# Kernel tuning notes

Hardware: AMD Instinct MI355X
Metric: run time of the kernel (lower is better)

Reference implementation:

```python
import jax, jax.numpy as jnp
import numpy as np

B, N, D, H, C = 32, 512, 256, 256, 2
EPS_NEIGH = 0.3
VSN = 1e-12
SMOOTH_R, DEGREE_R, SPARSITY_R = 0.2, 0.0, 0.1


def setup_inputs() -> dict:
    key = jax.random.key(0)
    ks = jax.random.split(key, 12)
    s = 0.02
    return {
        "context": jax.random.normal(ks[0], (B, N, D), jnp.float32),
        "attention_mask": jnp.ones((B, N, 1), jnp.int32),
        "W_gcn": jax.random.normal(ks[1], (D, H), jnp.float32) * s,
        "b_gcn": jnp.zeros((H,), jnp.float32),
        "W_att1": jax.random.normal(ks[2], (H, H), jnp.float32) * s,
        "b_att1": jnp.zeros((H,), jnp.float32),
        "ln_g": jnp.ones((H,), jnp.float32),
        "ln_b": jnp.zeros((H,), jnp.float32),
        "W_att2": jax.random.normal(ks[3], (H, 1), jnp.float32) * s,
        "b_att2": jnp.zeros((1,), jnp.float32),
        "W_out": jax.random.normal(ks[4], (H, C), jnp.float32) * s,
        "b_out": jnp.zeros((C,), jnp.float32),
    }


def reference(context, attention_mask, W_gcn, b_gcn, W_att1, b_att1,
              ln_g, ln_b, W_att2, b_att2, W_out, b_out):
    # --- GraphLearner (cosine metric + epsilon neighbourhood) ---
    cn = context / jnp.maximum(
        jnp.linalg.norm(context, axis=-1, keepdims=True), VSN)
    att = jnp.einsum('bnd,bmd->bnm', cn, cn)              # [B,N,N]
    mask = jax.lax.stop_gradient((att > EPS_NEIGH).astype(att.dtype))
    adj = att * mask                                      # markoff_value = 0

    # --- GCN diffusion (row-normalized adjacency) ---
    row = adj.sum(-1, keepdims=True)                      # [B,N,1]
    adj_norm = adj / (row + VSN)
    h = jax.nn.relu(
        jnp.einsum('bnm,bmd->bnd', adj_norm, context) @ W_gcn + b_gcn)

    # --- AttentionNetPooling: Linear -> LayerNorm -> GELU -> Linear(1) ---
    a = h @ W_att1 + b_att1
    mu = a.mean(-1, keepdims=True)
    var = a.var(-1, keepdims=True)
    a = (a - mu) / jnp.sqrt(var + 1e-5) * ln_g + ln_b
    w = jax.nn.gelu(a, approximate=False) @ W_att2 + b_att2   # [B,N,1]
    w = jnp.where(attention_mask == 0, -jnp.inf, w)
    w = jax.nn.softmax(w, axis=1)
    pooled = jnp.sum(w * h, axis=1)                       # [B,H]
    logits = pooled @ W_out + b_out                       # [B,C]

    # --- add_batch_graph_loss (L = diag(rowsum) - adj, topk = N) ---
    Lx = row * context - jnp.einsum('bnm,bmd->bnd', adj, context)
    smooth = SMOOTH_R * jnp.mean(
        jnp.sum(context * Lx, axis=(-1, -2)) / (N * N))
    deg = -DEGREE_R * jnp.mean(
        jnp.sum(jnp.log(row[..., 0] + VSN), axis=-1) / N)
    sparsity = SPARSITY_R * jnp.sum(adj ** 2) / (N * N) / B
    graph_loss = smooth + deg + sparsity
    return logits, graph_loss
```

## Files before the change

kernel.cpp:

```cpp
#include <hip/hip_runtime.h>
#include <math.h>

#define NS 512
#define ND 256
#define LIST_CAP 32768u

typedef short short8 __attribute__((ext_vector_type(8)));
typedef float f32x16 __attribute__((ext_vector_type(16)));

__device__ __forceinline__ unsigned short bf16_rne(float x) {
  unsigned u = __float_as_uint(x);
  unsigned r = u + 0x7fffu + ((u >> 16) & 1u);
  return (unsigned short)(r >> 16);
}
__device__ __forceinline__ float bf16_tof(unsigned short h) {
  return __uint_as_float(((unsigned)h) << 16);
}
__device__ __forceinline__ void bsplit(float x, unsigned short& h, unsigned short& l) {
  h = bf16_rne(x);
  l = bf16_rne(x - bf16_tof(h));
}
__device__ __forceinline__ float wave_sum(float v) {
  v += __shfl_xor(v, 1);  v += __shfl_xor(v, 2);  v += __shfl_xor(v, 4);
  v += __shfl_xor(v, 8);  v += __shfl_xor(v, 16); v += __shfl_xor(v, 32);
  return v;
}


__device__ __forceinline__ void gload_lds16(const void* g, void* l) {
  __builtin_amdgcn_global_load_lds(
      (const __attribute__((address_space(1))) unsigned int*)g,
      (__attribute__((address_space(3))) unsigned int*)l, 16, 0, 0);
}

__device__ __forceinline__ void stage4(const unsigned short* __restrict__ hiA,
                                       const unsigned short* __restrict__ loA, int grA,
                                       const unsigned short* __restrict__ hiB,
                                       const unsigned short* __restrict__ loB, int grB,
                                       int k0, char* lds, int wid, int lane)
{
  #pragma unroll
  for (int q = 0; q < 2; ++q) {
    const int c = (q * 4 + wid) * 64 + lane;
    const int row = c >> 3;
    const int soff = ((c & 7) * 16) ^ ((row & 7) << 4);
    const int dest = (q * 4 + wid) * 1024;
    const size_t ga = (size_t)(grA + row) * ND + k0 + (soff >> 1);
    const size_t gb = (size_t)(grB + row) * ND + k0 + (soff >> 1);
    gload_lds16(hiA + ga, lds + dest);
    gload_lds16(loA + ga, lds + 8192 + dest);
    gload_lds16(hiB + gb, lds + 16384 + dest);
    gload_lds16(loB + gb, lds + 24576 + dest);
  }
}

#define SWZB(row, off) (((row) << 7) + (((off) ^ (((row) & 7) << 4))))

#define STEP_MFMA(lds, arow, brow) do { \
  _Pragma("unroll") \
  for (int ks = 0; ks < 4; ++ks) { \
    const int off = ks * 32 + hl * 16; \
    short8 ah = *(const short8*)((lds) + SWZB((arow), off)); \
    short8 al = *(const short8*)((lds) + 8192 + SWZB((arow), off)); \
    short8 bh = *(const short8*)((lds) + 16384 + SWZB((brow), off)); \
    short8 bl = *(const short8*)((lds) + 24576 + SWZB((brow), off)); \
    acc = __builtin_amdgcn_mfma_f32_32x32x16_bf16(ah, bh, acc, 0, 0, 0); \
    acc = __builtin_amdgcn_mfma_f32_32x32x16_bf16(ah, bl, acc, 0, 0, 0); \
    acc = __builtin_amdgcn_mfma_f32_32x32x16_bf16(al, bh, acc, 0, 0, 0); \
  } \
} while (0)

__global__ __launch_bounds__(256)
void k_prep(const float* __restrict__ ctx, const float* __restrict__ Wg,
            const float* __restrict__ Wa,
            float* __restrict__ nrm, float* __restrict__ nsq,
            unsigned short* __restrict__ cnhi, unsigned short* __restrict__ cnlo,
            unsigned short* __restrict__ wgthi, unsigned short* __restrict__ wgtlo,
            unsigned short* __restrict__ wathi, unsigned short* __restrict__ watlo,
            unsigned* __restrict__ cnt)
{
  if (blockIdx.x >= 4096) {
    int wb = blockIdx.x - 4096;
    int j = wb & 255, selA = wb >> 8;
    int k = threadIdx.x;
    if (wb == 0 && k == 0) *cnt = 0u;
    const float* W = selA ? Wa : Wg;
    unsigned short h, l;
    bsplit(W[k * ND + j], h, l);
    if (selA) { wathi[j * ND + k] = h; watlo[j * ND + k] = l; }
    else      { wgthi[j * ND + k] = h; wgtlo[j * ND + k] = l; }
    return;
  }
  int w = threadIdx.x >> 6, lane = threadIdx.x & 63;
  int g = blockIdx.x * 4 + w;
  float4 v = ((const float4*)ctx)[(size_t)g * 64 + lane];
  float ss = v.x*v.x + v.y*v.y + v.z*v.z + v.w*v.w;
  ss = wave_sum(ss);
  float n = sqrtf(ss);
  float rn = 1.f / fmaxf(n, 1e-12f);
  if (lane == 0) { nrm[g] = n; nsq[g] = ss; }
  ushort4 hi, lo;
  bsplit(v.x * rn, hi.x, lo.x);
  bsplit(v.y * rn, hi.y, lo.y);
  bsplit(v.z * rn, hi.z, lo.z);
  bsplit(v.w * rn, hi.w, lo.w);
  ((ushort4*)cnhi)[(size_t)g * 64 + lane] = hi;
  ((ushort4*)cnlo)[(size_t)g * 64 + lane] = lo;
}

__global__ __launch_bounds__(256, 4)
void k_gram2(const unsigned short* __restrict__ cnhi, const unsigned short* __restrict__ cnlo,
             const float* __restrict__ nrm,
             float* __restrict__ rowp, float* __restrict__ diag,
             float* __restrict__ pA2, float* __restrict__ pA3,
             unsigned* __restrict__ cnt, unsigned* __restrict__ keys,
             float* __restrict__ vals)
{
  __shared__ __align__(16) char lds[32768];
  __shared__ float s_row[2][64];
  __shared__ float s_col[2][64];
  __shared__ float sred[8];
  const int bx0 = blockIdx.x;
  const int bx = (bx0 & 7) * 144 + (bx0 >> 3);
  const int b = bx / 36;
  int rem = bx % 36, ti = 0;
  #pragma unroll
  for (int q = 0; q < 7; ++q) { if (rem >= 8 - ti) { rem -= 8 - ti; ++ti; } }
  const int tj = ti + rem;
  const bool diagT = (ti == tj);
  const int i0 = ti * 64, j0 = tj * 64;
  const int bB = b * NS;
  const int rbA = bB + i0, rbB = bB + j0;

  const int tid = threadIdx.x;
  const int lane = tid & 63, wid = tid >> 6;
  const int l31 = lane & 31, hl = lane >> 5;
  const int wr = wid >> 1, wc = wid & 1;
  const int arow = wr * 32 + l31;
  const int brow = wc * 32 + l31;

  f32x16 acc = {};
  #pragma unroll
  for (int t = 0; t < 4; ++t) {
    stage4(cnhi, cnlo, rbA, cnhi, cnlo, rbB, t * 64, lds, wid, lane);
    __syncthreads();
    STEP_MFMA(lds, arow, brow);
    __syncthreads();
  }

  const float nc = nrm[rbB + wc * 32 + l31];
  const int gcol = wc * 32 + l31;
  float a2 = 0.f, a3 = 0.f, colsum = 0.f;

  #pragma unroll
  for (int r = 0; r < 16; ++r) {
    const int rofs = (r & 3) + 8 * (r >> 2) + 4 * hl;
    const int grow = wr * 32 + rofs;
    const float nr = nrm[rbA + grow];
    float v = acc[r];
    float adj = (v > 0.3f) ? v : 0.f;
    float q2 = adj * adj;
    a3 += q2;
    a2 += q2 * nr * nc;
    colsum += adj;
    if (diagT) {
      if (grow == gcol) {
        diag[bB + i0 + grow] = adj;
      } else if (adj > 0.f) {
        unsigned idx = atomicAdd(cnt, 1u);
        if (idx < LIST_CAP) {
          keys[idx] = (unsigned)((bB + i0 + grow) * NS + (j0 + gcol));
          vals[idx] = adj;
        }
      }
    } else if (adj > 0.f) {
      unsigned idx = atomicAdd(cnt, 2u);
      if (idx < LIST_CAP) {
        keys[idx] = (unsigned)((bB + i0 + grow) * NS + (j0 + gcol));
        vals[idx] = adj;
      }
      if (idx + 1u < LIST_CAP) {
        keys[idx + 1u] = (unsigned)((bB + j0 + gcol) * NS + (i0 + grow));
        vals[idx + 1u] = adj;
      }
    }
    float rs = adj;
    rs += __shfl_xor(rs, 1); rs += __shfl_xor(rs, 2); rs += __shfl_xor(rs, 4);
    rs += __shfl_xor(rs, 8); rs += __shfl_xor(rs, 16);
    if (l31 == 0) s_row[wc][grow] = rs;
  }
  colsum += __shfl_xor(colsum, 32);
  if (!diagT && hl == 0) s_col[wr][gcol] = colsum;
  a2 = wave_sum(a2);
  a3 = wave_sum(a3);
  if (lane == 0) { sred[wid] = a2; sred[4 + wid] = a3; }
  __syncthreads();
  if (tid < 64) {
    rowp[tj * 16384 + rbA + tid] = s_row[0][tid] + s_row[1][tid];
    if (!diagT)
      rowp[ti * 16384 + rbB + tid] = s_col[0][tid] + s_col[1][tid];
  }
  if (tid == 0) {
    float f = diagT ? 1.f : 2.f;
    pA2[bx] = f * (sred[0] + sred[1] + sred[2] + sred[3]);
    pA3[bx] = f * (sred[4] + sred[5] + sred[6] + sred[7]);
  }
}

__global__ __launch_bounds__(256)
void k_mrow(const float* __restrict__ ctx, const float* __restrict__ rowp,
            const float* __restrict__ nsq, const float* __restrict__ diag,
            const unsigned* __restrict__ cnt, const unsigned* __restrict__ keys,
            const float* __restrict__ vals,
            unsigned short* __restrict__ Mhi, unsigned short* __restrict__ Mlo,
            float* __restrict__ pA1)
{
  __shared__ float sa[4];
  int tid = threadIdx.x, w = tid >> 6, lane = tid & 63;
  int g = blockIdx.x * 4 + w;
  float r = 0.f;
  #pragma unroll
  for (int s = 0; s < 8; ++s) r += rowp[s * 16384 + g];
  float rr = 1.f / (r + 1e-12f);
  float4 v = ((const float4*)ctx)[(size_t)g * 64 + lane];
  float s = diag[g] * rr;
  float mx = v.x * s, my = v.y * s, mz = v.z * s, mw = v.w * s;
  unsigned c = *cnt; if (c > LIST_CAP) c = LIST_CAP;
  for (unsigned e = 0; e < c; ++e) {
    unsigned key = keys[e];
    if ((key >> 9) == (unsigned)g) {
      float vv = vals[e] * rr;
      unsigned bm = ((unsigned)g & ~511u) | (key & 511u);
      float4 cv = ((const float4*)ctx)[(size_t)bm * 64 + lane];
      mx = fmaf(vv, cv.x, mx); my = fmaf(vv, cv.y, my);
      mz = fmaf(vv, cv.z, mz); mw = fmaf(vv, cv.w, mw);
    }
  }
  ushort4 hi, lo;
  bsplit(mx, hi.x, lo.x); bsplit(my, hi.y, lo.y);
  bsplit(mz, hi.z, lo.z); bsplit(mw, hi.w, lo.w);
  ((ushort4*)Mhi)[(size_t)g * 64 + lane] = hi;
  ((ushort4*)Mlo)[(size_t)g * 64 + lane] = lo;
  if (lane == 0) sa[w] = r * nsq[g];
  __syncthreads();
  if (tid == 0) pA1[blockIdx.x] = sa[0] + sa[1] + sa[2] + sa[3];
}

template<int MODE>
__global__ __launch_bounds__(256, 4)
void k_mm(const unsigned short* __restrict__ Ahi, const unsigned short* __restrict__ Alo,
          const unsigned short* __restrict__ Bthi, const unsigned short* __restrict__ Btlo,
          const float* __restrict__ bias, float* __restrict__ outf,
          unsigned short* __restrict__ Ohi, unsigned short* __restrict__ Olo)
{
  __shared__ __align__(16) char lds[32768];
  const int i0 = blockIdx.x * 64;
  const int c0 = blockIdx.y * 64;
  const int tid = threadIdx.x;
  const int lane = tid & 63, wid = tid >> 6;
  const int l31 = lane & 31, hl = lane >> 5;
  const int wr = wid >> 1, wc = wid & 1;
  const int arow = wr * 32 + l31;
  const int brow = wc * 32 + l31;

  f32x16 acc = {};
  #pragma unroll
  for (int t = 0; t < 4; ++t) {
    stage4(Ahi, Alo, i0, Bthi, Btlo, c0, t * 64, lds, wid, lane);
    __syncthreads();
    STEP_MFMA(lds, arow, brow);
    __syncthreads();
  }

  const int gcol = c0 + wc * 32 + l31;
  const float bv = bias[gcol];
  #pragma unroll
  for (int r = 0; r < 16; ++r) {
    const int rofs = (r & 3) + 8 * (r >> 2) + 4 * hl;
    const size_t grow = (size_t)(i0 + wr * 32 + rofs);
    float v = acc[r] + bv;
    if (MODE == 0) {
      v = fmaxf(v, 0.f);
      unsigned short h, l;
      bsplit(v, h, l);
      Ohi[grow * ND + gcol] = h;
      Olo[grow * ND + gcol] = l;
    } else {
      outf[grow * ND + gcol] = v;
    }
  }
}

__global__ __launch_bounds__(256)
void k_ln(const float* __restrict__ a, const float* __restrict__ g,
          const float* __restrict__ bt, const float* __restrict__ W2,
          const float* __restrict__ b2, float* __restrict__ wl)
{
  int w = threadIdx.x >> 6, lane = threadIdx.x & 63;
  int row = blockIdx.x * 4 + w;
  float4 x = ((const float4*)a)[(size_t)row * 64 + lane];
  float s = x.x + x.y + x.z + x.w;
  float ss = fmaf(x.x, x.x, fmaf(x.y, x.y, fmaf(x.z, x.z, x.w * x.w)));
  s = wave_sum(s); ss = wave_sum(ss);
  float mu = s * (1.f / 256.f);
  float var = ss * (1.f / 256.f) - mu * mu;
  float rstd = rsqrtf(fmaxf(var, 0.f) + 1e-5f);
  float4 gg = ((const float4*)g)[lane];
  float4 bb = ((const float4*)bt)[lane];
  float4 wv = ((const float4*)W2)[lane];
  const float inv_sqrt2 = 0.70710678118654752f;
  float d = 0.f;
  float y = (x.x - mu) * rstd * gg.x + bb.x;
  d = fmaf(0.5f * y * (1.f + erff(y * inv_sqrt2)), wv.x, d);
  y = (x.y - mu) * rstd * gg.y + bb.y;
  d = fmaf(0.5f * y * (1.f + erff(y * inv_sqrt2)), wv.y, d);
  y = (x.z - mu) * rstd * gg.z + bb.z;
  d = fmaf(0.5f * y * (1.f + erff(y * inv_sqrt2)), wv.z, d);
  y = (x.w - mu) * rstd * gg.w + bb.w;
  d = fmaf(0.5f * y * (1.f + erff(y * inv_sqrt2)), wv.w, d);
  d = wave_sum(d);
  if (lane == 0) wl[row] = d + b2[0];
}

__global__ __launch_bounds__(256)
void k_pool2(const float* __restrict__ wl, const int* __restrict__ amask,
             const unsigned short* __restrict__ hhi, const unsigned short* __restrict__ hlo,
             float* __restrict__ part)
{
  __shared__ float sw[512];
  __shared__ float red[256];
  int b = blockIdx.x >> 4, p = blockIdx.x & 15, t = threadIdx.x;
  float l0 = (amask[b * NS + t]       == 0) ? -INFINITY : wl[b * NS + t];
  float l1 = (amask[b * NS + 256 + t] == 0) ? -INFINITY : wl[b * NS + 256 + t];
  red[t] = fmaxf(l0, l1);
  __syncthreads();
  for (int s = 128; s; s >>= 1) { if (t < s) red[t] = fmaxf(red[t], red[t + s]); __syncthreads(); }
  float mx = red[0];
  __syncthreads();
  float e0 = expf(l0 - mx), e1 = expf(l1 - mx);
  red[t] = e0 + e1;
  __syncthreads();
  for (int s = 128; s; s >>= 1) { if (t < s) red[t] += red[t + s]; __syncthreads(); }
  float inv = 1.f / red[0];
  sw[t] = e0 * inv; sw[256 + t] = e1 * inv;
  __syncthreads();
  const size_t base = (size_t)b * NS * ND + (size_t)p * 32 * ND + t;
  float acc = 0.f;
  #pragma unroll 8
  for (int n = 0; n < 32; ++n) {
    float hv = bf16_tof(hhi[base + (size_t)n * ND]) + bf16_tof(hlo[base + (size_t)n * ND]);
    acc = fmaf(sw[p * 32 + n], hv, acc);
  }
  part[(size_t)blockIdx.x * ND + t] = acc;
}

__global__ __launch_bounds__(256)
void k_final(const float* __restrict__ part, const float* __restrict__ W_out,
             const float* __restrict__ b_out, const float* __restrict__ pA1,
             const float* __restrict__ pA2, const float* __restrict__ pA3,
             float* __restrict__ out)
{
  __shared__ float red[512];
  int t = threadIdx.x;
  if (blockIdx.x < 32) {
    int b = blockIdx.x;
    float pl = 0.f;
    #pragma unroll
    for (int p = 0; p < 16; ++p) pl += part[(size_t)(b * 16 + p) * ND + t];
    red[t]       = pl * W_out[t * 2 + 0];
    red[256 + t] = pl * W_out[t * 2 + 1];
    __syncthreads();
    for (int s = 128; s; s >>= 1) {
      if (t < s) { red[t] += red[t + s]; red[256 + t] += red[256 + t + s]; }
      __syncthreads();
    }
    if (t == 0) {
      out[b * 2 + 0] = red[0]   + b_out[0];
      out[b * 2 + 1] = red[256] + b_out[1];
    }
  } else {
    float r1 = 0.f;
    #pragma unroll
    for (int i = 0; i < 16; ++i) r1 += pA1[i * 256 + t];
    float r2 = 0.f, r3 = 0.f;
    #pragma unroll
    for (int i = 0; i < 5; ++i) {
      int idx = i * 256 + t;
      if (idx < 1152) { r2 += pA2[idx]; r3 += pA3[idx]; }
    }
    red[t] = r1; red[256 + t] = r2;
    __syncthreads();
    for (int s = 128; s; s >>= 1) {
      if (t < s) { red[t] += red[t + s]; red[256 + t] += red[256 + t + s]; }
      __syncthreads();
    }
    r1 = red[0]; r2 = red[256];
    __syncthreads();
    red[t] = r3;
    __syncthreads();
    for (int s = 128; s; s >>= 1) { if (t < s) red[t] += red[t + s]; __syncthreads(); }
    if (t == 0) {
      float smooth = 0.2f * (r1 - r2) * (1.f / (32.f * 512.f * 512.f));
      float spars  = 0.1f * red[0] * (1.f / (512.f * 512.f)) * (1.f / 32.f);
      out[64] = smooth + spars;
    }
  }
}

extern "C" void kernel_launch(void* const* d_in, const int* in_sizes, int n_in,
                              void* d_out, int out_size, void* d_ws, size_t ws_size,
                              hipStream_t stream)
{
  (void)in_sizes; (void)n_in; (void)out_size; (void)ws_size;
  const float* ctx    = (const float*)d_in[0];
  const int*   amask  = (const int*)d_in[1];
  const float* W_gcn  = (const float*)d_in[2];
  const float* b_gcn  = (const float*)d_in[3];
  const float* W_att1 = (const float*)d_in[4];
  const float* b_att1 = (const float*)d_in[5];
  const float* ln_g   = (const float*)d_in[6];
  const float* ln_b   = (const float*)d_in[7];
  const float* W_att2 = (const float*)d_in[8];
  const float* b_att2 = (const float*)d_in[9];
  const float* W_out  = (const float*)d_in[10];
  const float* b_out  = (const float*)d_in[11];
  float* out = (float*)d_out;

  float* ws = (float*)d_ws;
  unsigned short* cnhi = (unsigned short*)ws;
  unsigned short* cnlo = (unsigned short*)(ws + 2097152);
  unsigned short* hhi  = cnhi;
  unsigned short* hlo  = cnlo;
  float* part = ws + 4194304;
  unsigned short* Mhi = (unsigned short*)(ws + 8388608);
  unsigned short* Mlo = (unsigned short*)(ws + 8388608 + 2097152);
  float* abuf = ws + 8388608;
  float* sp   = ws + 12582912;
  float* nrm  = sp;            sp += 16384;
  float* nsq  = sp;            sp += 16384;
  float* rowp = sp;            sp += 131072;
  float* diag = sp;            sp += 16384;
  float* wl   = sp;            sp += 16384;
  float* pA1  = sp;            sp += 4096;
  float* pA2  = sp;            sp += 1280;
  float* pA3  = sp;            sp += 1280;
  unsigned* cnt  = (unsigned*)sp;  sp += 64;
  unsigned* keys = (unsigned*)sp;  sp += 32768;
  float* vals = sp;            sp += 32768;
  unsigned short* wgthi = (unsigned short*)sp; sp += 32768;
  unsigned short* wgtlo = (unsigned short*)sp; sp += 32768;
  unsigned short* wathi = (unsigned short*)sp; sp += 32768;
  unsigned short* watlo = (unsigned short*)sp; sp += 32768;

  k_prep<<<4608, 256, 0, stream>>>(ctx, W_gcn, W_att1, nrm, nsq, cnhi, cnlo,
                                   wgthi, wgtlo, wathi, watlo, cnt);
  k_gram2<<<1152, 256, 0, stream>>>(cnhi, cnlo, nrm, rowp, diag, pA2, pA3,
                                    cnt, keys, vals);
  k_mrow<<<4096, 256, 0, stream>>>(ctx, rowp, nsq, diag, cnt, keys, vals,
                                   Mhi, Mlo, pA1);
  k_mm<0><<<dim3(256, 4), 256, 0, stream>>>(Mhi, Mlo, wgthi, wgtlo, b_gcn,
                                            nullptr, hhi, hlo);
  k_mm<1><<<dim3(256, 4), 256, 0, stream>>>(hhi, hlo, wathi, watlo, b_att1,
                                            abuf, nullptr, nullptr);
  k_ln<<<4096, 256, 0, stream>>>(abuf, ln_g, ln_b, W_att2, b_att2, wl);
  k_pool2<<<512, 256, 0, stream>>>(wl, amask, hhi, hlo, part);
  k_final<<<33, 256, 0, stream>>>(part, W_out, b_out, pA1, pA2, pA3, out);
}
```

Baseline: 84.88 us.

## Fuse diffusion into GCN GEMM, fuse attention GEMM with LayerNorm, merge pooling

The separate row-mixing kernel is removed. The GCN GEMM now runs directly on the normalized context and scales each row by norm*diag/rowsum, relying on the adjacency being diagonal-dominant. Rows that have off-diagonal neighbours are recomputed exactly in the attention kernel with a scalar dot-product fixup. The attention Linear, LayerNorm, GELU and Linear(1) are fused into one kernel using a pre-swizzled W_att1 fragment layout, and pooling is merged with the final reduction. Together these cut five launches and intermediate buffers down to three kernels. The costs are a serial, quadratic scan of the neighbour list in every attention block and a pooling stage with only 33 blocks.

```diff
diff --git a/kernel.cpp b/kernel.cpp
--- a/kernel.cpp
+++ b/kernel.cpp
@@ -25,7 +25,6 @@
   v += __shfl_xor(v, 8);  v += __shfl_xor(v, 16); v += __shfl_xor(v, 32);
   return v;
 }
-
 
 __device__ __forceinline__ void gload_lds16(const void* g, void* l) {
   __builtin_amdgcn_global_load_lds(
@@ -70,13 +69,23 @@
   } \
 } while (0)
 
+__device__ __forceinline__ float pdot_raw(const float* __restrict__ ctx,
+                                          const float* __restrict__ Wg,
+                                          int row, int t) {
+  const float* cr = ctx + (size_t)row * ND;
+  float a = 0.f;
+  #pragma unroll 4
+  for (int k = 0; k < ND; ++k) a = fmaf(cr[k], Wg[(size_t)k * ND + t], a);
+  return a;
+}
+
 __global__ __launch_bounds__(256)
 void k_prep(const float* __restrict__ ctx, const float* __restrict__ Wg,
             const float* __restrict__ Wa,
             float* __restrict__ nrm, float* __restrict__ nsq,
             unsigned short* __restrict__ cnhi, unsigned short* __restrict__ cnlo,
             unsigned short* __restrict__ wgthi, unsigned short* __restrict__ wgtlo,
-            unsigned short* __restrict__ wathi, unsigned short* __restrict__ watlo,
+            unsigned short* __restrict__ wfhi, unsigned short* __restrict__ wflo,
             unsigned* __restrict__ cnt)
 {
   if (blockIdx.x >= 4096) {
@@ -84,11 +93,15 @@
     int j = wb & 255, selA = wb >> 8;
     int k = threadIdx.x;
     if (wb == 0 && k == 0) *cnt = 0u;
-    const float* W = selA ? Wa : Wg;
     unsigned short h, l;
-    bsplit(W[k * ND + j], h, l);
-    if (selA) { wathi[j * ND + k] = h; watlo[j * ND + k] = l; }
-    else      { wgthi[j * ND + k] = h; wgtlo[j * ND + k] = l; }
+    if (selA) {
+      bsplit(Wa[k * ND + j], h, l);
+      int idx = ((((k >> 4) * 8) + (j >> 5)) * 64 + ((k >> 3) & 1) * 32 + (j & 31)) * 8 + (k & 7);
+      wfhi[idx] = h; wflo[idx] = l;
+    } else {
+      bsplit(Wg[k * ND + j], h, l);
+      wgthi[j * ND + k] = h; wgtlo[j * ND + k] = l;
+    }
     return;
   }
   int w = threadIdx.x >> 6, lane = threadIdx.x & 63;
@@ -207,53 +220,17 @@
   }
 }
 
-__global__ __launch_bounds__(256)
-void k_mrow(const float* __restrict__ ctx, const float* __restrict__ rowp,
-            const float* __restrict__ nsq, const float* __restrict__ diag,
-            const unsigned* __restrict__ cnt, const unsigned* __restrict__ keys,
-            const float* __restrict__ vals,
-            unsigned short* __restrict__ Mhi, unsigned short* __restrict__ Mlo,
-            float* __restrict__ pA1)
-{
-  __shared__ float sa[4];
-  int tid = threadIdx.x, w = tid >> 6, lane = tid & 63;
-  int g = blockIdx.x * 4 + w;
-  float r = 0.f;
-  #pragma unroll
-  for (int s = 0; s < 8; ++s) r += rowp[s * 16384 + g];
-  float rr = 1.f / (r + 1e-12f);
-  float4 v = ((const float4*)ctx)[(size_t)g * 64 + lane];
-  float s = diag[g] * rr;
-  float mx = v.x * s, my = v.y * s, mz = v.z * s, mw = v.w * s;
-  unsigned c = *cnt; if (c > LIST_CAP) c = LIST_CAP;
-  for (unsigned e = 0; e < c; ++e) {
-    unsigned key = keys[e];
-    if ((key >> 9) == (unsigned)g) {
-      float vv = vals[e] * rr;
-      unsigned bm = ((unsigned)g & ~511u) | (key & 511u);
-      float4 cv = ((const float4*)ctx)[(size_t)bm * 64 + lane];
-      mx = fmaf(vv, cv.x, mx); my = fmaf(vv, cv.y, my);
-      mz = fmaf(vv, cv.z, mz); mw = fmaf(vv, cv.w, mw);
-    }
-  }
-  ushort4 hi, lo;
-  bsplit(mx, hi.x, lo.x); bsplit(my, hi.y, lo.y);
-  bsplit(mz, hi.z, lo.z); bsplit(mw, hi.w, lo.w);
-  ((ushort4*)Mhi)[(size_t)g * 64 + lane] = hi;
-  ((ushort4*)Mlo)[(size_t)g * 64 + lane] = lo;
-  if (lane == 0) sa[w] = r * nsq[g];
-  __syncthreads();
-  if (tid == 0) pA1[blockIdx.x] = sa[0] + sa[1] + sa[2] + sa[3];
-}
-
-template<int MODE>
 __global__ __launch_bounds__(256, 4)
-void k_mm(const unsigned short* __restrict__ Ahi, const unsigned short* __restrict__ Alo,
-          const unsigned short* __restrict__ Bthi, const unsigned short* __restrict__ Btlo,
-          const float* __restrict__ bias, float* __restrict__ outf,
-          unsigned short* __restrict__ Ohi, unsigned short* __restrict__ Olo)
+void k_pgemm(const unsigned short* __restrict__ cnhi, const unsigned short* __restrict__ cnlo,
+             const unsigned short* __restrict__ wgthi, const unsigned short* __restrict__ wgtlo,
+             const float* __restrict__ rowp, const float* __restrict__ nrm,
+             const float* __restrict__ nsq, const float* __restrict__ diag,
+             const float* __restrict__ b_gcn,
+             unsigned short* __restrict__ Hhi, unsigned short* __restrict__ Hlo,
+             float* __restrict__ pA1)
 {
   __shared__ __align__(16) char lds[32768];
+  __shared__ float lss[64];
   const int i0 = blockIdx.x * 64;
   const int c0 = blockIdx.y * 64;
   const int tid = threadIdx.x;
@@ -263,142 +240,250 @@
   const int arow = wr * 32 + l31;
   const int brow = wc * 32 + l31;
 
+  if (tid < 64) {
+    int g = i0 + tid;
+    float r = 0.f;
+    #pragma unroll
+    for (int s2 = 0; s2 < 8; ++s2) r += rowp[s2 * 16384 + g];
+    float rr = 1.f / (r + 1e-12f);
+    lss[tid] = nrm[g] * diag[g] * rr;
+    float v = r * nsq[g];
+    v = wave_sum(v);
+    if (tid == 0 && blockIdx.y == 0) pA1[blockIdx.x] = v;
+  }
+
   f32x16 acc = {};
   #pragma unroll
   for (int t = 0; t < 4; ++t) {
-    stage4(Ahi, Alo, i0, Bthi, Btlo, c0, t * 64, lds, wid, lane);
+    stage4(cnhi, cnlo, i0, wgthi, wgtlo, c0, t * 64, lds, wid, lane);
     __syncthreads();
     STEP_MFMA(lds, arow, brow);
     __syncthreads();
   }
 
   const int gcol = c0 + wc * 32 + l31;
-  const float bv = bias[gcol];
+  const float bv = b_gcn[gcol];
   #pragma unroll
   for (int r = 0; r < 16; ++r) {
     const int rofs = (r & 3) + 8 * (r >> 2) + 4 * hl;
-    const size_t grow = (size_t)(i0 + wr * 32 + rofs);
-    float v = acc[r] + bv;
-    if (MODE == 0) {
-      v = fmaxf(v, 0.f);
-      unsigned short h, l;
-      bsplit(v, h, l);
-      Ohi[grow * ND + gcol] = h;
-      Olo[grow * ND + gcol] = l;
-    } else {
-      outf[grow * ND + gcol] = v;
-    }
-  }
-}
-
-__global__ __launch_bounds__(256)
-void k_ln(const float* __restrict__ a, const float* __restrict__ g,
-          const float* __restrict__ bt, const float* __restrict__ W2,
-          const float* __restrict__ b2, float* __restrict__ wl)
-{
-  int w = threadIdx.x >> 6, lane = threadIdx.x & 63;
-  int row = blockIdx.x * 4 + w;
-  float4 x = ((const float4*)a)[(size_t)row * 64 + lane];
-  float s = x.x + x.y + x.z + x.w;
-  float ss = fmaf(x.x, x.x, fmaf(x.y, x.y, fmaf(x.z, x.z, x.w * x.w)));
-  s = wave_sum(s); ss = wave_sum(ss);
-  float mu = s * (1.f / 256.f);
-  float var = ss * (1.f / 256.f) - mu * mu;
-  float rstd = rsqrtf(fmaxf(var, 0.f) + 1e-5f);
-  float4 gg = ((const float4*)g)[lane];
-  float4 bb = ((const float4*)bt)[lane];
-  float4 wv = ((const float4*)W2)[lane];
-  const float inv_sqrt2 = 0.70710678118654752f;
-  float d = 0.f;
-  float y = (x.x - mu) * rstd * gg.x + bb.x;
-  d = fmaf(0.5f * y * (1.f + erff(y * inv_sqrt2)), wv.x, d);
-  y = (x.y - mu) * rstd * gg.y + bb.y;
-  d = fmaf(0.5f * y * (1.f + erff(y * inv_sqrt2)), wv.y, d);
-  y = (x.z - mu) * rstd * gg.z + bb.z;
-  d = fmaf(0.5f * y * (1.f + erff(y * inv_sqrt2)), wv.z, d);
-  y = (x.w - mu) * rstd * gg.w + bb.w;
-  d = fmaf(0.5f * y * (1.f + erff(y * inv_sqrt2)), wv.w, d);
-  d = wave_sum(d);
-  if (lane == 0) wl[row] = d + b2[0];
-}
-
-__global__ __launch_bounds__(256)
-void k_pool2(const float* __restrict__ wl, const int* __restrict__ amask,
-             const unsigned short* __restrict__ hhi, const unsigned short* __restrict__ hlo,
-             float* __restrict__ part)
-{
+    const int lrow = wr * 32 + rofs;
+    const size_t grow = (size_t)(i0 + lrow);
+    float v = fmaxf(lss[lrow] * acc[r] + bv, 0.f);
+    unsigned short h, l;
+    bsplit(v, h, l);
+    Hhi[grow * ND + gcol] = h;
+    Hlo[grow * ND + gcol] = l;
+  }
+}
+
+__global__ __launch_bounds__(512)
+void k_att(unsigned short* __restrict__ Hhi, unsigned short* __restrict__ Hlo,
+           const unsigned short* __restrict__ wfhi, const unsigned short* __restrict__ wflo,
+           const float* __restrict__ ctx, const float* __restrict__ Wg,
+           const float* __restrict__ rowp, const float* __restrict__ diag,
+           const float* __restrict__ b_gcn,
+           const unsigned* __restrict__ cnt, const unsigned* __restrict__ keys,
+           const float* __restrict__ vals,
+           const float* __restrict__ b_att1, const float* __restrict__ ln_g,
+           const float* __restrict__ ln_b, const float* __restrict__ W2,
+           const float* __restrict__ b2, float* __restrict__ wl)
+{
+  __shared__ __align__(16) char lds[16384];
+  __shared__ float lnS[64][8], lnQ[64][8];
+  __shared__ float lmu[64], lrs[64];
+  __shared__ float wpart[64][8];
+  const int i0 = blockIdx.x * 64;
+  const int tid = threadIdx.x;
+  const int lane = tid & 63, wid = tid >> 6;
+  const int l31 = lane & 31, hl = lane >> 5;
+
+  unsigned c = *cnt; if (c > LIST_CAP) c = LIST_CAP;
+  for (unsigned e = 0; e < c; ++e) {
+    int bn = (int)(keys[e] >> 9);
+    if (bn < i0 || bn >= i0 + 64) continue;
+    bool first = true;
+    for (unsigned e2 = 0; e2 < e; ++e2)
+      if ((int)(keys[e2] >> 9) == bn) { first = false; break; }
+    if (!first) continue;
+    if (tid < 256) {
+      float r = 0.f;
+      #pragma unroll
+      for (int s2 = 0; s2 < 8; ++s2) r += rowp[s2 * 16384 + bn];
+      float rr = 1.f / (r + 1e-12f);
+      float pre = diag[bn] * rr * pdot_raw(ctx, Wg, bn, tid) + b_gcn[tid];
+      for (unsigned e2 = e; e2 < c; ++e2) {
+        unsigned k2 = keys[e2];
+        if ((int)(k2 >> 9) != bn) continue;
+        int bm = (bn & ~511) | (int)(k2 & 511u);
+        pre += vals[e2] * rr * pdot_raw(ctx, Wg, bm, tid);
+      }
+      float hv = fmaxf(pre, 0.f);
+      unsigned short hh, ll;
+      bsplit(hv, hh, ll);
+      Hhi[(size_t)bn * ND + tid] = hh;
+      Hlo[(size_t)bn * ND + tid] = ll;
+    }
+  }
+  __syncthreads();
+
+  f32x16 a0 = {}, a1 = {};
+  #pragma unroll
+  for (int t = 0; t < 4; ++t) {
+    {
+      const int cch = tid;
+      const int row = cch >> 3;
+      const int soff = ((cch & 7) * 16) ^ ((row & 7) << 4);
+      const int dest = wid * 1024;
+      const size_t ga = (size_t)(i0 + row) * ND + t * 64 + (soff >> 1);
+      gload_lds16(Hhi + ga, lds + dest);
+      gload_lds16(Hlo + ga, lds + 8192 + dest);
+    }
+    __syncthreads();
+    #pragma unroll
+    for (int ks = 0; ks < 4; ++ks) {
+      const int off = ks * 32 + hl * 16;
+      short8 ah0 = *(const short8*)(lds + SWZB(l31, off));
+      short8 ah1 = *(const short8*)(lds + SWZB(32 + l31, off));
+      short8 al0 = *(const short8*)(lds + 8192 + SWZB(l31, off));
+      short8 al1 = *(const short8*)(lds + 8192 + SWZB(32 + l31, off));
+      const size_t bidx = ((size_t)((t * 4 + ks) * 8 + wid) * 64 + lane) * 8;
+      short8 bh = *(const short8*)(wfhi + bidx);
+      short8 bl = *(const short8*)(wflo + bidx);
+      a0 = __builtin_amdgcn_mfma_f32_32x32x16_bf16(ah0, bh, a0, 0, 0, 0);
+      a0 = __builtin_amdgcn_mfma_f32_32x32x16_bf16(ah0, bl, a0, 0, 0, 0);
+      a0 = __builtin_amdgcn_mfma_f32_32x32x16_bf16(al0, bh, a0, 0, 0, 0);
+      a1 = __builtin_amdgcn_mfma_f32_32x32x16_bf16(ah1, bh, a1, 0, 0, 0);
+      a1 = __builtin_amdgcn_mfma_f32_32x32x16_bf16(ah1, bl, a1, 0, 0, 0);
+      a1 = __builtin_amdgcn_mfma_f32_32x32x16_bf16(al1, bh, a1, 0, 0, 0);
+    }
+    __syncthreads();
+  }
+
+  const float bt = b_att1[wid * 32 + l31];
+  #pragma unroll
+  for (int r = 0; r < 16; ++r) {
+    const int rofs = (r & 3) + 8 * (r >> 2) + 4 * hl;
+    float av = a0[r] + bt;
+    float s1 = av, s2 = av * av;
+    s1 += __shfl_xor(s1, 1); s1 += __shfl_xor(s1, 2); s1 += __shfl_xor(s1, 4);
+    s1 += __shfl_xor(s1, 8); s1 += __shfl_xor(s1, 16);
+    s2 += __shfl_xor(s2, 1); s2 += __shfl_xor(s2, 2); s2 += __shfl_xor(s2, 4);
+    s2 += __shfl_xor(s2, 8); s2 += __shfl_xor(s2, 16);
+    if (l31 == 0) { lnS[rofs][wid] = s1; lnQ[rofs][wid] = s2; }
+    av = a1[r] + bt;
+    s1 = av; s2 = av * av;
+    s1 += __shfl_xor(s1, 1); s1 += __shfl_xor(s1, 2); s1 += __shfl_xor(s1, 4);
+    s1 += __shfl_xor(s1, 8); s1 += __shfl_xor(s1, 16);
+    s2 += __shfl_xor(s2, 1); s2 += __shfl_xor(s2, 2); s2 += __shfl_xor(s2, 4);
+    s2 += __shfl_xor(s2, 8); s2 += __shfl_xor(s2, 16);
+    if (l31 == 0) { lnS[32 + rofs][wid] = s1; lnQ[32 + rofs][wid] = s2; }
+  }
+  __syncthreads();
+  if (tid < 64) {
+    float S = 0.f, Q = 0.f;
+    #pragma unroll
+    for (int w = 0; w < 8; ++w) { S += lnS[tid][w]; Q += lnQ[tid][w]; }
+    float mu = S * (1.f / 256.f);
+    float var = Q * (1.f / 256.f) - mu * mu;
+    lmu[tid] = mu;
+    lrs[tid] = rsqrtf(fmaxf(var, 0.f) + 1e-5f);
+  }
+  __syncthreads();
+
+  const float gg = ln_g[wid * 32 + l31];
+  const float gb = ln_b[wid * 32 + l31];
+  const float w2 = W2[wid * 32 + l31];
+  const float IS2 = 0.70710678118654752f;
+  #pragma unroll
+  for (int r = 0; r < 16; ++r) {
+    const int rofs = (r & 3) + 8 * (r >> 2) + 4 * hl;
+    float y = (a0[r] + bt - lmu[rofs]) * lrs[rofs] * gg + gb;
+    float d = 0.5f * y * (1.f + erff(y * IS2)) * w2;
+    d += __shfl_xor(d, 1); d += __shfl_xor(d, 2); d += __shfl_xor(d, 4);
+    d += __shfl_xor(d, 8); d += __shfl_xor(d, 16);
+    if (l31 == 0) wpart[rofs][wid] = d;
+    y = (a1[r] + bt - lmu[32 + rofs]) * lrs[32 + rofs] * gg + gb;
+    d = 0.5f * y * (1.f + erff(y * IS2)) * w2;
+    d += __shfl_xor(d, 1); d += __shfl_xor(d, 2); d += __shfl_xor(d, 4);
+    d += __shfl_xor(d, 8); d += __shfl_xor(d, 16);
+    if (l31 == 0) wpart[32 + rofs][wid] = d;
+  }
+  __syncthreads();
+  if (tid < 64) {
+    float d = 0.f;
+    #pragma unroll
+    for (int w = 0; w < 8; ++w) d += wpart[tid][w];
+    wl[i0 + tid] = d + b2[0];
+  }
+}
+
+__global__ __launch_bounds__(512)
+void k_poolfin(const float* __restrict__ wl, const int* __restrict__ amask,
+               const unsigned short* __restrict__ Hhi, const unsigned short* __restrict__ Hlo,
+               const float* __restrict__ W_out, const float* __restrict__ b_out,
+               const float* __restrict__ pA1, const float* __restrict__ pA2,
+               const float* __restrict__ pA3, float* __restrict__ out)
+{
+  __shared__ float red[512];
   __shared__ float sw[512];
-  __shared__ float red[256];
-  int b = blockIdx.x >> 4, p = blockIdx.x & 15, t = threadIdx.x;
-  float l0 = (amask[b * NS + t]       == 0) ? -INFINITY : wl[b * NS + t];
-  float l1 = (amask[b * NS + 256 + t] == 0) ? -INFINITY : wl[b * NS + 256 + t];
-  red[t] = fmaxf(l0, l1);
-  __syncthreads();
-  for (int s = 128; s; s >>= 1) { if (t < s) red[t] = fmaxf(red[t], red[t + s]); __syncthreads(); }
-  float mx = red[0];
-  __syncthreads();
-  float e0 = expf(l0 - mx), e1 = expf(l1 - mx);
-  red[t] = e0 + e1;
-  __syncthreads();
-  for (int s = 128; s; s >>= 1) { if (t < s) red[t] += red[t + s]; __syncthreads(); }
-  float inv = 1.f / red[0];
-  sw[t] = e0 * inv; sw[256 + t] = e1 * inv;
-  __syncthreads();
-  const size_t base = (size_t)b * NS * ND + (size_t)p * 32 * ND + t;
-  float acc = 0.f;
-  #pragma unroll 8
-  for (int n = 0; n < 32; ++n) {
-    float hv = bf16_tof(hhi[base + (size_t)n * ND]) + bf16_tof(hlo[base + (size_t)n * ND]);
-    acc = fmaf(sw[p * 32 + n], hv, acc);
-  }
-  part[(size_t)blockIdx.x * ND + t] = acc;
-}
-
-__global__ __launch_bounds__(256)
-void k_final(const float* __restrict__ part, const float* __restrict__ W_out,
-             const float* __restrict__ b_out, const float* __restrict__ pA1,
-             const float* __restrict__ pA2, const float* __restrict__ pA3,
-             float* __restrict__ out)
-{
-  __shared__ float red[512];
-  int t = threadIdx.x;
+  __shared__ float pp[512];
+  const int t = threadIdx.x;
   if (blockIdx.x < 32) {
-    int b = blockIdx.x;
-    float pl = 0.f;
-    #pragma unroll
-    for (int p = 0; p < 16; ++p) pl += part[(size_t)(b * 16 + p) * ND + t];
-    red[t]       = pl * W_out[t * 2 + 0];
-    red[256 + t] = pl * W_out[t * 2 + 1];
+    const int b = blockIdx.x;
+    float l = (amask[b * NS + t] == 0) ? -INFINITY : wl[b * NS + t];
+    red[t] = l;
+    __syncthreads();
+    for (int s = 256; s; s >>= 1) { if (t < s) red[t] = fmaxf(red[t], red[t + s]); __syncthreads(); }
+    float mx = red[0];
+    __syncthreads();
+    float e = expf(l - mx);
+    red[t] = e;
+    __syncthreads();
+    for (int s = 256; s; s >>= 1) { if (t < s) red[t] += red[t + s]; __syncthreads(); }
+    float inv = 1.f / red[0];
+    sw[t] = e * inv;
+    __syncthreads();
+    const int col = t & 255, half = t >> 8;
+    const size_t hb = ((size_t)b * NS + (size_t)half * 256) * ND + col;
+    float acc = 0.f;
+    #pragma unroll 8
+    for (int n = 0; n < 256; ++n) {
+      float hv = bf16_tof(Hhi[hb + (size_t)n * ND]) + bf16_tof(Hlo[hb + (size_t)n * ND]);
+      acc = fmaf(sw[half * 256 + n], hv, acc);
+    }
+    pp[t] = acc;
+    __syncthreads();
+    if (t < 256) {
+      float pool = pp[t] + pp[256 + t];
+      red[t] = pool * W_out[t * 2 + 0];
+      red[256 + t] = pool * W_out[t * 2 + 1];
+    }
     __syncthreads();
     for (int s = 128; s; s >>= 1) {
       if (t < s) { red[t] += red[t + s]; red[256 + t] += red[256 + t + s]; }
       __syncthreads();
     }
     if (t == 0) {
-      out[b * 2 + 0] = red[0]   + b_out[0];
+      out[b * 2 + 0] = red[0] + b_out[0];
       out[b * 2 + 1] = red[256] + b_out[1];
     }
   } else {
-    float r1 = 0.f;
-    #pragma unroll
-    for (int i = 0; i < 16; ++i) r1 += pA1[i * 256 + t];
-    float r2 = 0.f, r3 = 0.f;
-    #pragma unroll
-    for (int i = 0; i < 5; ++i) {
-      int idx = i * 256 + t;
-      if (idx < 1152) { r2 += pA2[idx]; r3 += pA3[idx]; }
-    }
-    red[t] = r1; red[256 + t] = r2;
-    __syncthreads();
-    for (int s = 128; s; s >>= 1) {
-      if (t < s) { red[t] += red[t + s]; red[256 + t] += red[256 + t + s]; }
-      __syncthreads();
-    }
-    r1 = red[0]; r2 = red[256];
+    float r1 = (t < 256) ? pA1[t] : 0.f;
+    float r2 = pA2[t] + pA2[512 + t] + ((t < 128) ? pA2[1024 + t] : 0.f);
+    float r3 = pA3[t] + pA3[512 + t] + ((t < 128) ? pA3[1024 + t] : 0.f);
+    red[t] = r1;
+    __syncthreads();
+    for (int s = 256; s; s >>= 1) { if (t < s) red[t] += red[t + s]; __syncthreads(); }
+    r1 = red[0];
+    __syncthreads();
+    red[t] = r2;
+    __syncthreads();
+    for (int s = 256; s; s >>= 1) { if (t < s) red[t] += red[t + s]; __syncthreads(); }
+    r2 = red[0];
     __syncthreads();
     red[t] = r3;
     __syncthreads();
-    for (int s = 128; s; s >>= 1) { if (t < s) red[t] += red[t + s]; __syncthreads(); }
+    for (int s = 256; s; s >>= 1) { if (t < s) red[t] += red[t + s]; __syncthreads(); }
     if (t == 0) {
       float smooth = 0.2f * (r1 - r2) * (1.f / (32.f * 512.f * 512.f));
       float spars  = 0.1f * red[0] * (1.f / (512.f * 512.f)) * (1.f / 32.f);
@@ -429,12 +514,8 @@
   float* ws = (float*)d_ws;
   unsigned short* cnhi = (unsigned short*)ws;
   unsigned short* cnlo = (unsigned short*)(ws + 2097152);
-  unsigned short* hhi  = cnhi;
-  unsigned short* hlo  = cnlo;
-  float* part = ws + 4194304;
-  unsigned short* Mhi = (unsigned short*)(ws + 8388608);
-  unsigned short* Mlo = (unsigned short*)(ws + 8388608 + 2097152);
-  float* abuf = ws + 8388608;
+  unsigned short* Hhi  = (unsigned short*)(ws + 4194304);
+  unsigned short* Hlo  = (unsigned short*)(ws + 4194304 + 2097152);
   float* sp   = ws + 12582912;
   float* nrm  = sp;            sp += 16384;
   float* nsq  = sp;            sp += 16384;
@@ -449,20 +530,18 @@
   float* vals = sp;            sp += 32768;
   unsigned short* wgthi = (unsigned short*)sp; sp += 32768;
   unsigned short* wgtlo = (unsigned short*)sp; sp += 32768;
-  unsigned short* wathi = (unsigned short*)sp; sp += 32768;
-  unsigned short* watlo = (unsigned short*)sp; sp += 32768;
+  unsigned short* wfhi  = (unsigned short*)sp; sp += 32768;
+  unsigned short* wflo  = (unsigned short*)sp; sp += 32768;
 
   k_prep<<<4608, 256, 0, stream>>>(ctx, W_gcn, W_att1, nrm, nsq, cnhi, cnlo,
-                                   wgthi, wgtlo, wathi, watlo, cnt);
+                                   wgthi, wgtlo, wfhi, wflo, cnt);
   k_gram2<<<1152, 256, 0, stream>>>(cnhi, cnlo, nrm, rowp, diag, pA2, pA3,
                                     cnt, keys, vals);
-  k_mrow<<<4096, 256, 0, stream>>>(ctx, rowp, nsq, diag, cnt, keys, vals,
-                                   Mhi, Mlo, pA1);
-  k_mm<0><<<dim3(256, 4), 256, 0, stream>>>(Mhi, Mlo, wgthi, wgtlo, b_gcn,
-                                            nullptr, hhi, hlo);
-  k_mm<1><<<dim3(256, 4), 256, 0, stream>>>(hhi, hlo, wathi, watlo, b_att1,
-                                            abuf, nullptr, nullptr);
-  k_ln<<<4096, 256, 0, stream>>>(abuf, ln_g, ln_b, W_att2, b_att2, wl);
-  k_pool2<<<512, 256, 0, stream>>>(wl, amask, hhi, hlo, part);
-  k_final<<<33, 256, 0, stream>>>(part, W_out, b_out, pA1, pA2, pA3, out);
-}
+  k_pgemm<<<dim3(256, 4), 256, 0, stream>>>(cnhi, cnlo, wgthi, wgtlo, rowp,
+                                            nrm, nsq, diag, b_gcn, Hhi, Hlo, pA1);
+  k_att<<<256, 512, 0, stream>>>(Hhi, Hlo, wfhi, wflo, ctx, W_gcn, rowp, diag,
+                                 b_gcn, cnt, keys, vals, b_att1, ln_g, ln_b,
+                                 W_att2, b_att2, wl);
+  k_poolfin<<<33, 512, 0, stream>>>(wl, amask, Hhi, Hlo, W_out, b_out,
+                                    pA1, pA2, pA3, out);
+}
```

New measurement: 118.3 us. +39.4%, slower.
